# Kernel tuning notes

Measured on AMD Instinct MI355X. Metric: run time of the kernel, lower is better.

The kernel has to match this reference:

```python
import jax, jax.numpy as jnp
import numpy as np

M_BLOCK = 8  # N:M group size along in_features

def nm_mask(shape, m):
    """Deterministic VENOM mask from VenomSparsifier.get_random_mask:
    keep positions 0 and 2 in every m-sized group along the last dim."""
    pat = np.zeros(m, dtype=np.float32)
    pat[0] = 1.0
    pat[2] = 1.0
    mask = np.tile(pat, shape[-1] // m)  # [in_features]
    return jnp.asarray(np.broadcast_to(mask, shape))

def setup_inputs() -> dict:
    key = jax.random.key(0)
    k1, k2, k3 = jax.random.split(key, 3)
    B, S, D_IN, D_OUT = 4, 4096, 4096, 4096
    x = jax.random.normal(k1, (B, S, D_IN), dtype=jnp.float32)
    weight = jax.random.normal(k2, (D_OUT, D_IN), dtype=jnp.float32) * 0.02
    bias = jax.random.normal(k3, (D_OUT,), dtype=jnp.float32) * 0.02
    return {"x": x, "weight": weight, "bias": bias}

def reference(x, weight, bias):
    # Structured-sparse linear: y = x @ (W * mask).T + b
    w_sp = weight * nm_mask(weight.shape, M_BLOCK)  # [out, in], 2:8 sparse
    out = jnp.einsum('bsk,nk->bsn', x, w_sp) + bias  # [B, S, out]
    return out
```

## Files before the change

### kernel.cpp

```cpp
#include <hip/hip_runtime.h>
#include <stdint.h>


typedef __attribute__((ext_vector_type(8))) short short8;
typedef __attribute__((ext_vector_type(4))) float float4_t;

typedef unsigned short u16;
typedef unsigned int   u32;

#define M_TOT 16384
#define N_TOT 4096
#define K_ACT 4096
#define K_C   1024
#define NT    16

typedef __attribute__((address_space(1))) void GlobVoid;
typedef __attribute__((address_space(3))) void LdsVoid;

static __device__ __forceinline__ u32 f32_to_bf16_rne(float f) {
    u32 u = __float_as_uint(f);
    u32 rounded = u + 0x7FFFu + ((u >> 16) & 1u);
    return rounded >> 16;
}

__global__ __launch_bounds__(256) void compact_k(const float4* __restrict__ src,
                                                 u32* __restrict__ dst, int n) {
    int i = blockIdx.x * 256 + threadIdx.x;
    if (i >= n) return;
    float4 g = src[(size_t)i * 2];
    dst[i] = f32_to_bf16_rne(g.x) | (f32_to_bf16_rne(g.z) << 16);
}

static __device__ __forceinline__ void stage_half(const u16* __restrict__ src,
                                                  int row0, int kt,
                                                  u16* lds_half,
                                                  int wave, int lane) {
#pragma unroll
    for (int c = 0; c < 2; ++c) {
        const int blk = c * 8 + wave;
        const int r   = blk * 8 + (lane >> 3);
        const int cb  = (lane & 7) * 16;
        const int cbs = cb ^ ((r & 4) << 3);
        const u16* g = src + (size_t)(row0 + r) * K_C + kt * 64 + (cbs >> 1);
        __builtin_amdgcn_global_load_lds((GlobVoid*)g,
                                         (LdsVoid*)(lds_half + blk * 512),
                                         16, 0, 0);
    }
}


#define PHASE(ABASE, BBASE, MH, NH, STAGE_STMT, VMCNT_STMT)                     \
    do {                                                                        \
        short8 afr[4][2], bfr[2][2];                                            \
        const u16* Ah = lds + (ABASE);                                          \
        const u16* Bh = lds + (BBASE);                                          \
        _Pragma("unroll")                                                       \
        for (int i = 0; i < 4; ++i) {                                           \
            afr[i][0] = *(const short8*)(Ah + arow + i * 1024 + ck0);           \
            afr[i][1] = *(const short8*)(Ah + arow + i * 1024 + ck1);           \
        }                                                                       \
        _Pragma("unroll")                                                       \
        for (int j = 0; j < 2; ++j) {                                           \
            bfr[j][0] = *(const short8*)(Bh + brow + j * 1024 + ck0);           \
            bfr[j][1] = *(const short8*)(Bh + brow + j * 1024 + ck1);           \
        }                                                                       \
        STAGE_STMT;                                                             \
        __builtin_amdgcn_s_barrier();                                           \
        asm volatile("s_waitcnt lgkmcnt(0)" ::: "memory");                      \
        __builtin_amdgcn_sched_barrier(0);                                      \
        __builtin_amdgcn_s_setprio(1);                                          \
        _Pragma("unroll")                                                       \
        for (int i = 0; i < 4; ++i) {                                           \
            _Pragma("unroll")                                                   \
            for (int j = 0; j < 2; ++j) {                                       \
                acc[MH][NH][i][j] = __builtin_amdgcn_mfma_f32_16x16x32_bf16(    \
                    afr[i][0], bfr[j][0], acc[MH][NH][i][j], 0, 0, 0);          \
                acc[MH][NH][i][j] = __builtin_amdgcn_mfma_f32_16x16x32_bf16(    \
                    afr[i][1], bfr[j][1], acc[MH][NH][i][j], 0, 0, 0);          \
            }                                                                   \
        }                                                                       \
        __builtin_amdgcn_s_setprio(0);                                          \
        VMCNT_STMT;                                                             \
        __builtin_amdgcn_s_barrier();                                           \
    } while (0)

__global__ __launch_bounds__(512, 2) void gemm_bt(const u16* __restrict__ A,
                                                  const u16* __restrict__ B,
                                                  const float* __restrict__ bias,
                                                  float* __restrict__ C) {
    __shared__ u16 lds[65536];

    const int tid  = threadIdx.x;
    const int lane = tid & 63;
    const int wave = tid >> 6;
    const int wm   = wave >> 2;
    const int wn   = wave & 3;
    const int fr   = lane & 15;
    const int q    = lane >> 4;

    const int wg  = blockIdx.x;
    const int swz = (wg & 7) * 128 + (wg >> 3);
    const int m0  = (swz >> 4) * 256;
    const int n0  = (swz & 15) * 256;

    const int ck0 = (((0 * 64) + q * 16) ^ ((fr & 4) << 3)) >> 1;
    const int ck1 = (((1 * 64) + q * 16) ^ ((fr & 4) << 3)) >> 1;
    const int arow = (wm * 64 + fr) * 64;
    const int brow = (wn * 32 + fr) * 64;

    float4_t acc[2][2][4][2];
    const float4_t fzero = {0.f, 0.f, 0.f, 0.f};
#pragma unroll
    for (int mh = 0; mh < 2; ++mh)
#pragma unroll
        for (int nh = 0; nh < 2; ++nh)
#pragma unroll
            for (int i = 0; i < 4; ++i)
#pragma unroll
                for (int j = 0; j < 2; ++j) acc[mh][nh][i][j] = fzero;

    stage_half(A, m0 + 0,   0, lds + 0,     wave, lane);
    stage_half(B, n0 + 0,   0, lds + 16384, wave, lane);
    stage_half(A, m0 + 128, 0, lds + 8192,  wave, lane);
    stage_half(B, n0 + 128, 0, lds + 24576, wave, lane);
    stage_half(A, m0 + 0,   1, lds + 32768, wave, lane);
    stage_half(B, n0 + 0,   1, lds + 49152, wave, lane);
    asm volatile("s_waitcnt vmcnt(4)" ::: "memory");
    __builtin_amdgcn_s_barrier();

    for (int it = 0; it < NT / 2; ++it) {
        const int u  = 2 * it;
        const int t1 = u + 1;
        const int t2 = (u + 2 < NT) ? u + 2 : NT - 1;
        const int t3 = (u + 3 < NT) ? u + 3 : NT - 1;

        PHASE(0, 16384, 0, 0,
              stage_half(A, m0 + 128, t1, lds + 40960, wave, lane), ((void)0));
        PHASE(0, 24576, 0, 1,
              stage_half(B, n0 + 128, t1, lds + 57344, wave, lane), ((void)0));
        PHASE(8192, 16384, 1, 0,
              stage_half(A, m0 + 0, t2, lds + 0, wave, lane), ((void)0));
        PHASE(8192, 24576, 1, 1,
              stage_half(B, n0 + 0, t2, lds + 16384, wave, lane),
              asm volatile("s_waitcnt vmcnt(4)" ::: "memory"));
        PHASE(32768, 49152, 0, 0,
              stage_half(A, m0 + 128, t2, lds + 8192, wave, lane), ((void)0));
        PHASE(32768, 57344, 0, 1,
              stage_half(B, n0 + 128, t2, lds + 24576, wave, lane), ((void)0));
        PHASE(40960, 49152, 1, 0,
              stage_half(A, m0 + 0, t3, lds + 32768, wave, lane), ((void)0));
        PHASE(40960, 57344, 1, 1,
              stage_half(B, n0 + 0, t3, lds + 49152, wave, lane),
              asm volatile("s_waitcnt vmcnt(4)" ::: "memory"));
    }

    const int rq = (lane >> 4) * 4;
#pragma unroll
    for (int nh = 0; nh < 2; ++nh) {
#pragma unroll
        for (int j = 0; j < 2; ++j) {
            const int col  = n0 + nh * 128 + wn * 32 + j * 16 + fr;
            const float bj = bias[col];
#pragma unroll
            for (int mh = 0; mh < 2; ++mh) {
#pragma unroll
                for (int i = 0; i < 4; ++i) {
                    const int row = m0 + mh * 128 + wm * 64 + i * 16 + rq;
#pragma unroll
                    for (int r = 0; r < 4; ++r) {
                        C[(size_t)(row + r) * N_TOT + col] = acc[mh][nh][i][j][r] + bj;
                    }
                }
            }
        }
    }
}

__global__ __launch_bounds__(256) void fallback_k(const float* __restrict__ X,
                                                  const float* __restrict__ W,
                                                  const float* __restrict__ bias,
                                                  float* __restrict__ out) {
    size_t idx = (size_t)blockIdx.x * 256 + threadIdx.x;
    int n    = (int)(idx & (N_TOT - 1));
    size_t m = idx >> 12;
    const float* xr = X + m * K_ACT;
    const float* wr = W + (size_t)n * K_ACT;
    float acc = 0.f;
    for (int g = 0; g < K_ACT / 8; ++g) {
        acc += xr[g * 8] * wr[g * 8] + xr[g * 8 + 2] * wr[g * 8 + 2];
    }
    out[idx] = acc + bias[n];
}

extern "C" void kernel_launch(void* const* d_in, const int* in_sizes, int n_in,
                              void* d_out, int out_size, void* d_ws, size_t ws_size,
                              hipStream_t stream) {
    const float* x    = (const float*)d_in[0];
    const float* w    = (const float*)d_in[1];
    const float* bias = (const float*)d_in[2];
    float* out = (float*)d_out;

    const size_t xc_elems = (size_t)M_TOT * K_C;
    const size_t wc_elems = (size_t)N_TOT * K_C;
    const size_t need = (xc_elems + wc_elems) * sizeof(u16);

    if (ws_size >= need) {
        u16* xc = (u16*)d_ws;
        u16* wc = xc + xc_elems;

        const int ngx = M_TOT * (K_ACT / 8);
        const int ngw = N_TOT * (K_ACT / 8);
        compact_k<<<ngx / 256, 256, 0, stream>>>((const float4*)x, (u32*)xc, ngx);
        compact_k<<<ngw / 256, 256, 0, stream>>>((const float4*)w, (u32*)wc, ngw);

        gemm_bt<<<dim3(1024), dim3(512), 0, stream>>>(xc, wc, bias, out);
    } else {
        const size_t total = (size_t)M_TOT * N_TOT;
        fallback_k<<<(int)(total / 256), 256, 0, stream>>>(x, w, bias, out);
    }
}
```

Measured before the change: 639.2 us.

## Reorder GEMM phases to reuse B fragments and change LDS swizzle

After: 612.4 us. 1.04x faster.

```diff
diff --git a/kernel.cpp b/kernel.cpp
--- a/kernel.cpp
+++ b/kernel.cpp
@@ -40,7 +40,7 @@
         const int blk = c * 8 + wave;
         const int r   = blk * 8 + (lane >> 3);
         const int cb  = (lane & 7) * 16;
-        const int cbs = cb ^ ((r & 4) << 3);
+        const int cbs = cb ^ ((r & 3) << 5);
         const u16* g = src + (size_t)(row0 + r) * K_C + kt * 64 + (cbs >> 1);
         __builtin_amdgcn_global_load_lds((GlobVoid*)g,
                                          (LdsVoid*)(lds_half + blk * 512),
@@ -49,22 +49,26 @@
 }
 
 
-#define PHASE(ABASE, BBASE, MH, NH, STAGE_STMT, VMCNT_STMT)                     \
+#define LOAD_AFR(HBASE)                                                         \
     do {                                                                        \
-        short8 afr[4][2], bfr[2][2];                                            \
-        const u16* Ah = lds + (ABASE);                                          \
-        const u16* Bh = lds + (BBASE);                                          \
         _Pragma("unroll")                                                       \
         for (int i = 0; i < 4; ++i) {                                           \
-            afr[i][0] = *(const short8*)(Ah + arow + i * 1024 + ck0);           \
-            afr[i][1] = *(const short8*)(Ah + arow + i * 1024 + ck1);           \
+            afr[i][0] = *(const short8*)(lds + (HBASE) + arow + i * 1024 + ck0);\
+            afr[i][1] = *(const short8*)(lds + (HBASE) + arow + i * 1024 + ck1);\
         }                                                                       \
+    } while (0)
+
+#define LOAD_BFR(HBASE, BF)                                                     \
+    do {                                                                        \
         _Pragma("unroll")                                                       \
         for (int j = 0; j < 2; ++j) {                                           \
-            bfr[j][0] = *(const short8*)(Bh + brow + j * 1024 + ck0);           \
-            bfr[j][1] = *(const short8*)(Bh + brow + j * 1024 + ck1);           \
+            BF[j][0] = *(const short8*)(lds + (HBASE) + brow + j * 1024 + ck0); \
+            BF[j][1] = *(const short8*)(lds + (HBASE) + brow + j * 1024 + ck1); \
         }                                                                       \
-        STAGE_STMT;                                                             \
+    } while (0)
+
+#define MFMA16(MH, NH, BF)                                                      \
+    do {                                                                        \
         __builtin_amdgcn_s_barrier();                                           \
         asm volatile("s_waitcnt lgkmcnt(0)" ::: "memory");                      \
         __builtin_amdgcn_sched_barrier(0);                                      \
@@ -74,14 +78,12 @@
             _Pragma("unroll")                                                   \
             for (int j = 0; j < 2; ++j) {                                       \
                 acc[MH][NH][i][j] = __builtin_amdgcn_mfma_f32_16x16x32_bf16(    \
-                    afr[i][0], bfr[j][0], acc[MH][NH][i][j], 0, 0, 0);          \
+                    afr[i][0], BF[j][0], acc[MH][NH][i][j], 0, 0, 0);           \
                 acc[MH][NH][i][j] = __builtin_amdgcn_mfma_f32_16x16x32_bf16(    \
-                    afr[i][1], bfr[j][1], acc[MH][NH][i][j], 0, 0, 0);          \
+                    afr[i][1], BF[j][1], acc[MH][NH][i][j], 0, 0, 0);           \
             }                                                                   \
         }                                                                       \
         __builtin_amdgcn_s_setprio(0);                                          \
-        VMCNT_STMT;                                                             \
-        __builtin_amdgcn_s_barrier();                                           \
     } while (0)
 
 __global__ __launch_bounds__(512, 2) void gemm_bt(const u16* __restrict__ A,
@@ -103,8 +105,8 @@
     const int m0  = (swz >> 4) * 256;
     const int n0  = (swz & 15) * 256;
 
-    const int ck0 = (((0 * 64) + q * 16) ^ ((fr & 4) << 3)) >> 1;
-    const int ck1 = (((1 * 64) + q * 16) ^ ((fr & 4) << 3)) >> 1;
+    const int ck0 = (((0 * 64) + q * 16) ^ ((fr & 3) << 5)) >> 1;
+    const int ck1 = (((1 * 64) + q * 16) ^ ((fr & 3) << 5)) >> 1;
     const int arow = (wm * 64 + fr) * 64;
     const int brow = (wn * 32 + fr) * 64;
 
@@ -119,12 +121,14 @@
 #pragma unroll
                 for (int j = 0; j < 2; ++j) acc[mh][nh][i][j] = fzero;
 
+    short8 afr[4][2], bfr0[2][2], bfr1[2][2];
+
     stage_half(A, m0 + 0,   0, lds + 0,     wave, lane);
+    stage_half(A, m0 + 128, 0, lds + 8192,  wave, lane);
     stage_half(B, n0 + 0,   0, lds + 16384, wave, lane);
-    stage_half(A, m0 + 128, 0, lds + 8192,  wave, lane);
     stage_half(B, n0 + 128, 0, lds + 24576, wave, lane);
-    stage_half(A, m0 + 0,   1, lds + 32768, wave, lane);
     stage_half(B, n0 + 0,   1, lds + 49152, wave, lane);
+    stage_half(B, n0 + 128, 1, lds + 57344, wave, lane);
     asm volatile("s_waitcnt vmcnt(4)" ::: "memory");
     __builtin_amdgcn_s_barrier();
 
@@ -134,25 +138,51 @@
         const int t2 = (u + 2 < NT) ? u + 2 : NT - 1;
         const int t3 = (u + 3 < NT) ? u + 3 : NT - 1;
 
-        PHASE(0, 16384, 0, 0,
-              stage_half(A, m0 + 128, t1, lds + 40960, wave, lane), ((void)0));
-        PHASE(0, 24576, 0, 1,
-              stage_half(B, n0 + 128, t1, lds + 57344, wave, lane), ((void)0));
-        PHASE(8192, 16384, 1, 0,
-              stage_half(A, m0 + 0, t2, lds + 0, wave, lane), ((void)0));
-        PHASE(8192, 24576, 1, 1,
-              stage_half(B, n0 + 0, t2, lds + 16384, wave, lane),
-              asm volatile("s_waitcnt vmcnt(4)" ::: "memory"));
-        PHASE(32768, 49152, 0, 0,
-              stage_half(A, m0 + 128, t2, lds + 8192, wave, lane), ((void)0));
-        PHASE(32768, 57344, 0, 1,
-              stage_half(B, n0 + 128, t2, lds + 24576, wave, lane), ((void)0));
-        PHASE(40960, 49152, 1, 0,
-              stage_half(A, m0 + 0, t3, lds + 32768, wave, lane), ((void)0));
-        PHASE(40960, 57344, 1, 1,
-              stage_half(B, n0 + 0, t3, lds + 49152, wave, lane),
-              asm volatile("s_waitcnt vmcnt(4)" ::: "memory"));
-    }
+        LOAD_AFR(0); LOAD_BFR(16384, bfr0);
+        stage_half(A, m0 + 0, t1, lds + 32768, wave, lane);
+        MFMA16(0, 0, bfr0);
+        __builtin_amdgcn_s_barrier();
+
+        LOAD_AFR(8192);
+        stage_half(A, m0 + 128, t1, lds + 40960, wave, lane);
+        MFMA16(1, 0, bfr0);
+        __builtin_amdgcn_s_barrier();
+
+        LOAD_BFR(24576, bfr1);
+        stage_half(B, n0 + 0, t2, lds + 16384, wave, lane);
+        MFMA16(1, 1, bfr1);
+        __builtin_amdgcn_s_barrier();
+
+        LOAD_AFR(0);
+        stage_half(B, n0 + 128, t2, lds + 24576, wave, lane);
+        MFMA16(0, 1, bfr1);
+        asm volatile("s_waitcnt vmcnt(4)" ::: "memory");
+        __builtin_amdgcn_s_barrier();
+
+        LOAD_AFR(32768); LOAD_BFR(49152, bfr0);
+        stage_half(A, m0 + 0, t2, lds + 0, wave, lane);
+        MFMA16(0, 0, bfr0);
+        __builtin_amdgcn_s_barrier();
+
+        LOAD_AFR(40960);
+        stage_half(A, m0 + 128, t2, lds + 8192, wave, lane);
+        MFMA16(1, 0, bfr0);
+        __builtin_amdgcn_s_barrier();
+
+        LOAD_BFR(57344, bfr1);
+        stage_half(B, n0 + 0, t3, lds + 49152, wave, lane);
+        MFMA16(1, 1, bfr1);
+        __builtin_amdgcn_s_barrier();
+
+        LOAD_AFR(32768);
+        stage_half(B, n0 + 128, t3, lds + 57344, wave, lane);
+        MFMA16(0, 1, bfr1);
+        asm volatile("s_waitcnt vmcnt(4)" ::: "memory");
+        __builtin_amdgcn_s_barrier();
+    }
+
+    asm volatile("s_waitcnt vmcnt(0)" ::: "memory");
+    __builtin_amdgcn_s_barrier();
 
     const int rq = (lane >> 4) * 4;
 #pragma unroll
```
